# Optimization experiments

Measured on AMD Instinct MI355X. Metric: run time of the kernel, lower is better.

## Reference

```python
import jax, jax.numpy as jnp
import numpy as np

N = 1_000_000
M = 8
HX = HY = 64
U = V = 512
L = 96 // 6  # latent_size // 6 = 16


def setup_inputs() -> dict:
    key = jax.random.key(0)
    ks = jax.random.split(key, 11)
    r = jax.random.uniform(ks[0], (N,), dtype=jnp.float32)
    m = jax.random.randint(ks[1], (N,), 0, M, dtype=jnp.int32)
    h = jax.random.uniform(ks[2], (N, 2), dtype=jnp.float32, minval=-1.0, maxval=1.0)
    u = jax.random.uniform(ks[3], (N,), dtype=jnp.float32)
    v = jax.random.uniform(ks[4], (N,), dtype=jnp.float32)
    Fxy = jax.random.normal(ks[5], (M, HX, HY, L), dtype=jnp.float32)
    Fxu = jax.random.normal(ks[6], (M, HX, U, L), dtype=jnp.float32)
    Fxv = jax.random.normal(ks[7], (M, HX, V, L), dtype=jnp.float32)
    Fyu = jax.random.normal(ks[8], (M, HY, U, L), dtype=jnp.float32)
    Fyv = jax.random.normal(ks[9], (M, HY, V, L), dtype=jnp.float32)
    Fuv = jax.random.normal(ks[10], (M, U, V, L), dtype=jnp.float32)
    return {"r": r, "m": m, "h": h, "u": u, "v": v,
            "Fxy": Fxy, "Fxu": Fxu, "Fxv": Fxv,
            "Fyu": Fyu, "Fyv": Fyv, "Fuv": Fuv}


def _bilinear(x, m, i, j, I, J):
    # x: [M, I, J, L]; m,i,j: [N]; wrap-around bilinear interpolation
    i1 = jnp.floor(i).astype(jnp.int32)
    j1 = jnp.floor(j).astype(jnp.int32)
    i2 = (i1 + 1) % I
    j2 = (j1 + 1) % J
    ir = (i - i1)[..., None]  # [N,1]
    jr = (j - j1)[..., None]
    top = x[m, i1, j1, :] * (1 - ir) + x[m, i2, j1, :] * ir
    bot = x[m, i1, j2, :] * (1 - ir) + x[m, i2, j2, :] * ir
    return top * (1 - jr) + bot * jr


def reference(r, m, h, u, v, Fxy, Fxu, Fxv, Fyu, Fyv, Fuv) -> jnp.ndarray:
    ind_hx = (h[..., 0] + 1) / 2 * HX
    ind_hy = (h[..., 1] + 1) / 2 * HY
    ind_hx = jnp.where(ind_hx == HX, HX - 1, ind_hx)
    ind_hy = jnp.where(ind_hy == HY, HY - 1, ind_hy)
    ind_u = u * U
    ind_v = v * V
    ind_u = jnp.where(ind_u == U, U - 1, ind_u)
    ind_v = jnp.where(ind_v == V, V - 1, ind_v)
    latent = jnp.concatenate([
        _bilinear(Fxy, m, ind_hx, ind_hy, HX, HY),
        _bilinear(Fxu, m, ind_hx, ind_u, HX, U),
        _bilinear(Fxv, m, ind_hx, ind_v, HX, V),
        _bilinear(Fyu, m, ind_hy, ind_u, HY, U),
        _bilinear(Fyv, m, ind_hy, ind_v, HY, V),
        _bilinear(Fuv, m, ind_u, ind_v, U, V),
    ], axis=-1)  # [N, 6*L]
    return latent
```

## Files before the change

kernel.cpp:

```cpp
#include <hip/hip_runtime.h>

#define HXc 64
#define HYc 64
#define Uc  512
#define Vc  512
#define Lc  16

typedef float v4f __attribute__((ext_vector_type(4)));
typedef float v2f __attribute__((ext_vector_type(2)));

struct BL {
    const float* a11;
    const float* a21;
    const float* a12;
    const float* a22;
    float ir, jr;
};

__device__ __forceinline__ v4f ld4(const float* p) {
    return *reinterpret_cast<const v4f*>(p);
}

__device__ __forceinline__ BL mk(const float* __restrict__ base, int mm,
                                 float fi, float fj, int I, int J, int chan) {
    BL b;
    int i1 = (int)floorf(fi);
    int j1 = (int)floorf(fj);
    b.ir = fi - (float)i1;
    b.jr = fj - (float)j1;
    int i2 = (i1 + 1 == I) ? 0 : (i1 + 1);
    int j2 = (j1 + 1 == J) ? 0 : (j1 + 1);
    const float* p = base + ((size_t)mm * I * J) * Lc + chan;
    b.a11 = p + (size_t)(i1 * J + j1) * Lc;
    b.a21 = p + (size_t)(i2 * J + j1) * Lc;
    b.a12 = p + (size_t)(i1 * J + j2) * Lc;
    b.a22 = p + (size_t)(i2 * J + j2) * Lc;
    return b;
}

__device__ __forceinline__ v4f blend(v4f c11, v4f c21, v4f c12, v4f c22,
                                     float ir, float jr) {
    float oir = 1.0f - ir;
    float ojr = 1.0f - jr;
    v4f top = c11 * oir + c21 * ir;
    v4f bot = c12 * oir + c22 * ir;
    return top * ojr + bot * jr;
}

__global__ __launch_bounds__(256) void triplane_kernel(
    const int*   __restrict__ m_arr,
    const float* __restrict__ h,
    const float* __restrict__ u_arr,
    const float* __restrict__ v_arr,
    const float* __restrict__ Fxy,
    const float* __restrict__ Fxu,
    const float* __restrict__ Fxv,
    const float* __restrict__ Fyu,
    const float* __restrict__ Fyv,
    const float* __restrict__ Fuv,
    float* __restrict__ out,
    int N)
{
    int tid = blockIdx.x * blockDim.x + threadIdx.x;
    int n   = tid >> 2;
    int sub = tid & 3;
    if (n >= N) return;

    v2f hh = __builtin_nontemporal_load(reinterpret_cast<const v2f*>(h) + n);
    float uu = __builtin_nontemporal_load(u_arr + n);
    float vv = __builtin_nontemporal_load(v_arr + n);
    int   mm = __builtin_nontemporal_load(m_arr + n);

    float ind_hx = (hh.x + 1.0f) * 0.5f * (float)HXc;
    float ind_hy = (hh.y + 1.0f) * 0.5f * (float)HYc;
    if (ind_hx == (float)HXc) ind_hx = (float)(HXc - 1);
    if (ind_hy == (float)HYc) ind_hy = (float)(HYc - 1);
    float ind_u = uu * (float)Uc;
    float ind_v = vv * (float)Vc;
    if (ind_u == (float)Uc) ind_u = (float)(Uc - 1);
    if (ind_v == (float)Vc) ind_v = (float)(Vc - 1);

    int chan = sub * 4;

    BL b0 = mk(Fxy, mm, ind_hx, ind_hy, HXc, HYc, chan);
    BL b1 = mk(Fxu, mm, ind_hx, ind_u,  HXc, Uc,  chan);
    BL b2 = mk(Fxv, mm, ind_hx, ind_v,  HXc, Vc,  chan);
    BL b3 = mk(Fyu, mm, ind_hy, ind_u,  HYc, Uc,  chan);
    BL b4 = mk(Fyv, mm, ind_hy, ind_v,  HYc, Vc,  chan);
    BL b5 = mk(Fuv, mm, ind_u,  ind_v,  Uc,  Vc,  chan);

    v4f c0a = ld4(b0.a11); v4f c0b = ld4(b0.a21); v4f c0c = ld4(b0.a12); v4f c0d = ld4(b0.a22);
    v4f c1a = ld4(b1.a11); v4f c1b = ld4(b1.a21); v4f c1c = ld4(b1.a12); v4f c1d = ld4(b1.a22);
    v4f c2a = ld4(b2.a11); v4f c2b = ld4(b2.a21); v4f c2c = ld4(b2.a12); v4f c2d = ld4(b2.a22);
    v4f c3a = ld4(b3.a11); v4f c3b = ld4(b3.a21); v4f c3c = ld4(b3.a12); v4f c3d = ld4(b3.a22);
    v4f c4a = ld4(b4.a11); v4f c4b = ld4(b4.a21); v4f c4c = ld4(b4.a12); v4f c4d = ld4(b4.a22);
    v4f c5a = ld4(b5.a11); v4f c5b = ld4(b5.a21); v4f c5c = ld4(b5.a12); v4f c5d = ld4(b5.a22);

    __builtin_amdgcn_sched_barrier(0);

    float* o = out + (size_t)n * 96 + chan;

    v4f r0 = blend(c0a, c0b, c0c, c0d, b0.ir, b0.jr);
    __builtin_nontemporal_store(r0, reinterpret_cast<v4f*>(o + 0 * Lc));
    v4f r1 = blend(c1a, c1b, c1c, c1d, b1.ir, b1.jr);
    __builtin_nontemporal_store(r1, reinterpret_cast<v4f*>(o + 1 * Lc));
    v4f r2 = blend(c2a, c2b, c2c, c2d, b2.ir, b2.jr);
    __builtin_nontemporal_store(r2, reinterpret_cast<v4f*>(o + 2 * Lc));
    v4f r3 = blend(c3a, c3b, c3c, c3d, b3.ir, b3.jr);
    __builtin_nontemporal_store(r3, reinterpret_cast<v4f*>(o + 3 * Lc));
    v4f r4 = blend(c4a, c4b, c4c, c4d, b4.ir, b4.jr);
    __builtin_nontemporal_store(r4, reinterpret_cast<v4f*>(o + 4 * Lc));
    v4f r5 = blend(c5a, c5b, c5c, c5d, b5.ir, b5.jr);
    __builtin_nontemporal_store(r5, reinterpret_cast<v4f*>(o + 5 * Lc));
}

extern "C" void kernel_launch(void* const* d_in, const int* in_sizes, int n_in,
                              void* d_out, int out_size, void* d_ws, size_t ws_size,
                              hipStream_t stream) {
    const int*   m_arr = (const int*)  d_in[1];
    const float* h     = (const float*)d_in[2];
    const float* u_arr = (const float*)d_in[3];
    const float* v_arr = (const float*)d_in[4];
    const float* Fxy   = (const float*)d_in[5];
    const float* Fxu   = (const float*)d_in[6];
    const float* Fxv   = (const float*)d_in[7];
    const float* Fyu   = (const float*)d_in[8];
    const float* Fyv   = (const float*)d_in[9];
    const float* Fuv   = (const float*)d_in[10];
    float* out = (float*)d_out;

    int N = in_sizes[0];
    int total_threads = 4 * N;
    dim3 block(256);
    dim3 grid((total_threads + 255) / 256);
    triplane_kernel<<<grid, block, 0, stream>>>(m_arr, h, u_arr, v_arr,
                                                Fxy, Fxu, Fxv, Fyu, Fyv, Fuv,
                                                out, N);
}
```

Measured before the change: 780.5 us.

## Bucket-sort points by (m,u,v) tile before gathering for cache locality

Adds a counting-sort pre-pass (zero, histogram, single-block scan, atomic scatter) that groups points by material and 16x16 (u,v) tile, then runs the bilinear gather over sorted points and writes results back through an index array. The goal is to raise L2/MALL hit rates for the large Fuv/Fxu/Fyu tables, whose random gathers dominate cost. It also applies an XCD-aware block swizzle so neighbouring sorted chunks land on the same XCD, and switches output stores from nontemporal to normal. In exchange it adds four extra launches, atomics on hot buckets, scattered output writes and about 24 bytes per point of workspace traffic. If the workspace is missing or too small, the code falls back to the original flat kernel.

```diff
diff --git a/kernel.cpp b/kernel.cpp
--- a/kernel.cpp
+++ b/kernel.cpp
@@ -5,15 +5,94 @@
 #define Uc  512
 #define Vc  512
 #define Lc  16
+#define NBUCK 8192
 
 typedef float v4f __attribute__((ext_vector_type(4)));
-typedef float v2f __attribute__((ext_vector_type(2)));
+
+
+__device__ __forceinline__ void compute_inds(float h0, float h1, float uu, float vv,
+                                             float& ix, float& iy, float& iu, float& iv) {
+    ix = (h0 + 1.0f) * 0.5f * (float)HXc; if (ix == (float)HXc) ix = (float)(HXc - 1);
+    iy = (h1 + 1.0f) * 0.5f * (float)HYc; if (iy == (float)HYc) iy = (float)(HYc - 1);
+    iu = uu * (float)Uc;                  if (iu == (float)Uc)  iu = (float)(Uc - 1);
+    iv = vv * (float)Vc;                  if (iv == (float)Vc)  iv = (float)(Vc - 1);
+}
+
+__device__ __forceinline__ int bucket_of(int mm, float iu, float iv) {
+    int us = ((int)iu) >> 4;
+    int vs = ((int)iv) >> 4;
+    return (((mm << 5) | vs) << 5) | us;
+}
+
+
+__global__ __launch_bounds__(256) void zero_kernel(int* __restrict__ counts) {
+    int i = blockIdx.x * 256 + threadIdx.x;
+    if (i < NBUCK) counts[i] = 0;
+}
+
+
+__global__ __launch_bounds__(256) void hist_kernel(
+    const int* __restrict__ m_arr, const float* __restrict__ u_arr,
+    const float* __restrict__ v_arr, int* __restrict__ counts, int N)
+{
+    int n = blockIdx.x * 256 + threadIdx.x;
+    if (n >= N) return;
+    float iu = u_arr[n] * (float)Uc; if (iu == (float)Uc) iu = (float)(Uc - 1);
+    float iv = v_arr[n] * (float)Vc; if (iv == (float)Vc) iv = (float)(Vc - 1);
+    atomicAdd(&counts[bucket_of(m_arr[n], iu, iv)], 1);
+}
+
+
+__global__ __launch_bounds__(1024) void scan_kernel(
+    const int* __restrict__ counts, int* __restrict__ cursors)
+{
+    __shared__ int lds[1024];
+    int t = threadIdx.x;
+    int base = t * 8;
+    int s = 0;
+    #pragma unroll
+    for (int k = 0; k < 8; ++k) s += counts[base + k];
+    lds[t] = s;
+    __syncthreads();
+    for (int off = 1; off < 1024; off <<= 1) {
+        int val = (t >= off) ? lds[t - off] : 0;
+        __syncthreads();
+        lds[t] += val;
+        __syncthreads();
+    }
+    int run = lds[t] - s;
+    #pragma unroll
+    for (int k = 0; k < 8; ++k) {
+        cursors[base + k] = run;
+        run += counts[base + k];
+    }
+}
+
+
+__global__ __launch_bounds__(256) void scatter_kernel(
+    const int* __restrict__ m_arr, const float* __restrict__ h,
+    const float* __restrict__ u_arr, const float* __restrict__ v_arr,
+    int* __restrict__ cursors,
+    v4f* __restrict__ inds4, int* __restrict__ m_s, int* __restrict__ outidx,
+    int N)
+{
+    int n = blockIdx.x * 256 + threadIdx.x;
+    if (n >= N) return;
+    float h0 = h[2 * n], h1 = h[2 * n + 1];
+    float ix, iy, iu, iv;
+    compute_inds(h0, h1, u_arr[n], v_arr[n], ix, iy, iu, iv);
+    int mm = m_arr[n];
+    int b  = bucket_of(mm, iu, iv);
+    int pos = atomicAdd(&cursors[b], 1);
+    v4f rec; rec.x = ix; rec.y = iy; rec.z = iu; rec.w = iv;
+    inds4[pos]  = rec;
+    m_s[pos]    = mm;
+    outidx[pos] = n;
+}
+
 
 struct BL {
-    const float* a11;
-    const float* a21;
-    const float* a12;
-    const float* a22;
+    const float* a11; const float* a21; const float* a12; const float* a22;
     float ir, jr;
 };
 
@@ -47,38 +126,28 @@
     return top * ojr + bot * jr;
 }
 
-__global__ __launch_bounds__(256) void triplane_kernel(
-    const int*   __restrict__ m_arr,
-    const float* __restrict__ h,
-    const float* __restrict__ u_arr,
-    const float* __restrict__ v_arr,
-    const float* __restrict__ Fxy,
-    const float* __restrict__ Fxu,
-    const float* __restrict__ Fxv,
-    const float* __restrict__ Fyu,
-    const float* __restrict__ Fyv,
-    const float* __restrict__ Fuv,
-    float* __restrict__ out,
-    int N)
-{
-    int tid = blockIdx.x * blockDim.x + threadIdx.x;
-    int n   = tid >> 2;
-    int sub = tid & 3;
-    if (n >= N) return;
-
-    v2f hh = __builtin_nontemporal_load(reinterpret_cast<const v2f*>(h) + n);
-    float uu = __builtin_nontemporal_load(u_arr + n);
-    float vv = __builtin_nontemporal_load(v_arr + n);
-    int   mm = __builtin_nontemporal_load(m_arr + n);
-
-    float ind_hx = (hh.x + 1.0f) * 0.5f * (float)HXc;
-    float ind_hy = (hh.y + 1.0f) * 0.5f * (float)HYc;
-    if (ind_hx == (float)HXc) ind_hx = (float)(HXc - 1);
-    if (ind_hy == (float)HYc) ind_hy = (float)(HYc - 1);
-    float ind_u = uu * (float)Uc;
-    float ind_v = vv * (float)Vc;
-    if (ind_u == (float)Uc) ind_u = (float)(Uc - 1);
-    if (ind_v == (float)Vc) ind_v = (float)(Vc - 1);
+__global__ __launch_bounds__(256) void main_kernel(
+    const v4f* __restrict__ inds4, const int* __restrict__ m_s,
+    const int* __restrict__ outidx,
+    const float* __restrict__ Fxy, const float* __restrict__ Fxu,
+    const float* __restrict__ Fxv, const float* __restrict__ Fyu,
+    const float* __restrict__ Fyv, const float* __restrict__ Fuv,
+    float* __restrict__ out, int N, int nwg)
+{
+    int bid = blockIdx.x;
+    int q = nwg >> 3, r = nwg & 7;
+    int xcd = bid & 7, idx = bid >> 3;
+    int swz = (xcd < r) ? (xcd * (q + 1) + idx) : (r * (q + 1) + (xcd - r) * q + idx);
+
+    int t   = swz * 256 + threadIdx.x;
+    int k   = t >> 2;
+    int sub = t & 3;
+    if (k >= N) return;
+
+    v4f inds = inds4[k];
+    int mm   = m_s[k];
+    int n    = outidx[k];
+    float ind_hx = inds.x, ind_hy = inds.y, ind_u = inds.z, ind_v = inds.w;
 
     int chan = sub * 4;
 
@@ -100,19 +169,61 @@
 
     float* o = out + (size_t)n * 96 + chan;
 
-    v4f r0 = blend(c0a, c0b, c0c, c0d, b0.ir, b0.jr);
-    __builtin_nontemporal_store(r0, reinterpret_cast<v4f*>(o + 0 * Lc));
-    v4f r1 = blend(c1a, c1b, c1c, c1d, b1.ir, b1.jr);
-    __builtin_nontemporal_store(r1, reinterpret_cast<v4f*>(o + 1 * Lc));
-    v4f r2 = blend(c2a, c2b, c2c, c2d, b2.ir, b2.jr);
-    __builtin_nontemporal_store(r2, reinterpret_cast<v4f*>(o + 2 * Lc));
-    v4f r3 = blend(c3a, c3b, c3c, c3d, b3.ir, b3.jr);
-    __builtin_nontemporal_store(r3, reinterpret_cast<v4f*>(o + 3 * Lc));
-    v4f r4 = blend(c4a, c4b, c4c, c4d, b4.ir, b4.jr);
-    __builtin_nontemporal_store(r4, reinterpret_cast<v4f*>(o + 4 * Lc));
-    v4f r5 = blend(c5a, c5b, c5c, c5d, b5.ir, b5.jr);
-    __builtin_nontemporal_store(r5, reinterpret_cast<v4f*>(o + 5 * Lc));
-}
+    *reinterpret_cast<v4f*>(o + 0 * Lc) = blend(c0a, c0b, c0c, c0d, b0.ir, b0.jr);
+    *reinterpret_cast<v4f*>(o + 1 * Lc) = blend(c1a, c1b, c1c, c1d, b1.ir, b1.jr);
+    *reinterpret_cast<v4f*>(o + 2 * Lc) = blend(c2a, c2b, c2c, c2d, b2.ir, b2.jr);
+    *reinterpret_cast<v4f*>(o + 3 * Lc) = blend(c3a, c3b, c3c, c3d, b3.ir, b3.jr);
+    *reinterpret_cast<v4f*>(o + 4 * Lc) = blend(c4a, c4b, c4c, c4d, b4.ir, b4.jr);
+    *reinterpret_cast<v4f*>(o + 5 * Lc) = blend(c5a, c5b, c5c, c5d, b5.ir, b5.jr);
+}
+
+
+__global__ __launch_bounds__(256) void flat_kernel(
+    const int*   __restrict__ m_arr,
+    const float* __restrict__ h,
+    const float* __restrict__ u_arr,
+    const float* __restrict__ v_arr,
+    const float* __restrict__ Fxy, const float* __restrict__ Fxu,
+    const float* __restrict__ Fxv, const float* __restrict__ Fyu,
+    const float* __restrict__ Fyv, const float* __restrict__ Fuv,
+    float* __restrict__ out, int N)
+{
+    int tid = blockIdx.x * blockDim.x + threadIdx.x;
+    int n   = tid >> 2;
+    int sub = tid & 3;
+    if (n >= N) return;
+
+    float h0 = h[2 * n], h1 = h[2 * n + 1];
+    float ind_hx, ind_hy, ind_u, ind_v;
+    compute_inds(h0, h1, u_arr[n], v_arr[n], ind_hx, ind_hy, ind_u, ind_v);
+    int mm = m_arr[n];
+    int chan = sub * 4;
+
+    BL b0 = mk(Fxy, mm, ind_hx, ind_hy, HXc, HYc, chan);
+    BL b1 = mk(Fxu, mm, ind_hx, ind_u,  HXc, Uc,  chan);
+    BL b2 = mk(Fxv, mm, ind_hx, ind_v,  HXc, Vc,  chan);
+    BL b3 = mk(Fyu, mm, ind_hy, ind_u,  HYc, Uc,  chan);
+    BL b4 = mk(Fyv, mm, ind_hy, ind_v,  HYc, Vc,  chan);
+    BL b5 = mk(Fuv, mm, ind_u,  ind_v,  Uc,  Vc,  chan);
+
+    v4f c0a = ld4(b0.a11); v4f c0b = ld4(b0.a21); v4f c0c = ld4(b0.a12); v4f c0d = ld4(b0.a22);
+    v4f c1a = ld4(b1.a11); v4f c1b = ld4(b1.a21); v4f c1c = ld4(b1.a12); v4f c1d = ld4(b1.a22);
+    v4f c2a = ld4(b2.a11); v4f c2b = ld4(b2.a21); v4f c2c = ld4(b2.a12); v4f c2d = ld4(b2.a22);
+    v4f c3a = ld4(b3.a11); v4f c3b = ld4(b3.a21); v4f c3c = ld4(b3.a12); v4f c3d = ld4(b3.a22);
+    v4f c4a = ld4(b4.a11); v4f c4b = ld4(b4.a21); v4f c4c = ld4(b4.a12); v4f c4d = ld4(b4.a22);
+    v4f c5a = ld4(b5.a11); v4f c5b = ld4(b5.a21); v4f c5c = ld4(b5.a12); v4f c5d = ld4(b5.a22);
+
+    __builtin_amdgcn_sched_barrier(0);
+
+    float* o = out + (size_t)n * 96 + chan;
+    *reinterpret_cast<v4f*>(o + 0 * Lc) = blend(c0a, c0b, c0c, c0d, b0.ir, b0.jr);
+    *reinterpret_cast<v4f*>(o + 1 * Lc) = blend(c1a, c1b, c1c, c1d, b1.ir, b1.jr);
+    *reinterpret_cast<v4f*>(o + 2 * Lc) = blend(c2a, c2b, c2c, c2d, b2.ir, b2.jr);
+    *reinterpret_cast<v4f*>(o + 3 * Lc) = blend(c3a, c3b, c3c, c3d, b3.ir, b3.jr);
+    *reinterpret_cast<v4f*>(o + 4 * Lc) = blend(c4a, c4b, c4c, c4d, b4.ir, b4.jr);
+    *reinterpret_cast<v4f*>(o + 5 * Lc) = blend(c5a, c5b, c5c, c5d, b5.ir, b5.jr);
+}
+
 
 extern "C" void kernel_launch(void* const* d_in, const int* in_sizes, int n_in,
                               void* d_out, int out_size, void* d_ws, size_t ws_size,
@@ -130,10 +241,42 @@
     float* out = (float*)d_out;
 
     int N = in_sizes[0];
+
+    size_t off_counts  = 0;
+    size_t off_cursors = off_counts  + (size_t)NBUCK * 4;
+    size_t off_inds4   = off_cursors + (size_t)NBUCK * 4;
+    size_t off_ms      = off_inds4   + (size_t)N * 16;
+    size_t off_outidx  = off_ms      + (size_t)N * 4;
+    size_t needed      = off_outidx  + (size_t)N * 4;
+
+    if (d_ws == nullptr || ws_size < needed) {
+        int total_threads = 4 * N;
+        dim3 block(256);
+        dim3 grid((total_threads + 255) / 256);
+        flat_kernel<<<grid, block, 0, stream>>>(m_arr, h, u_arr, v_arr,
+                                                Fxy, Fxu, Fxv, Fyu, Fyv, Fuv, out, N);
+        return;
+    }
+
+    char* ws = (char*)d_ws;
+    int* counts  = (int*)(ws + off_counts);
+    int* cursors = (int*)(ws + off_cursors);
+    v4f* inds4   = (v4f*)(ws + off_inds4);
+    int* m_s     = (int*)(ws + off_ms);
+    int* outidx  = (int*)(ws + off_outidx);
+
+    dim3 blk(256);
+    dim3 grdN((N + 255) / 256);
+
+    zero_kernel<<<dim3((NBUCK + 255) / 256), blk, 0, stream>>>(counts);
+    hist_kernel<<<grdN, blk, 0, stream>>>(m_arr, u_arr, v_arr, counts, N);
+    scan_kernel<<<dim3(1), dim3(1024), 0, stream>>>(counts, cursors);
+    scatter_kernel<<<grdN, blk, 0, stream>>>(m_arr, h, u_arr, v_arr, cursors,
+                                             inds4, m_s, outidx, N);
+
     int total_threads = 4 * N;
-    dim3 block(256);
-    dim3 grid((total_threads + 255) / 256);
-    triplane_kernel<<<grid, block, 0, stream>>>(m_arr, h, u_arr, v_arr,
-                                                Fxy, Fxu, Fxv, Fyu, Fyv, Fuv,
-                                                out, N);
-}
+    int nwg = (total_threads + 255) / 256;
+    main_kernel<<<dim3(nwg), blk, 0, stream>>>(inds4, m_s, outidx,
+                                               Fxy, Fxu, Fxv, Fyu, Fyv, Fuv,
+                                               out, N, nwg);
+}
```

Measured after the change: 787.2 us. About the same (+0.9%).
